# Kernel optimization log

Measured on AMD Instinct MI355X. Metric: run time of the kernel, lower is better.

## Reference

```python
import jax, jax.numpy as jnp
import numpy as np

B, C, H, NP, M = 32, 768, 12, 196, 64
D = C // H
GRID = 14  # sqrt(196)
NG = 1 + NP  # cls + patches = 197
EPS = 1e-5


def _ln(x, w, b):
    mu = x.mean(-1, keepdims=True)
    var = ((x - mu) ** 2).mean(-1, keepdims=True)
    return (x - mu) * jax.lax.rsqrt(var + EPS) * w + b


def setup_inputs() -> dict:
    key = jax.random.key(0)
    ks = jax.random.split(key, 14)
    std = 0.02
    return {
        "x": jax.random.normal(ks[0], (B, NG + M, C), dtype=jnp.float32),
        "ps": jax.random.uniform(ks[1], (B, M, 2), dtype=jnp.float32) * 224.0,
        "ns": jax.random.randint(ks[2], (B,), 1, M + 1, dtype=jnp.int32),
        "norm1_w": jnp.ones((C,), jnp.float32),
        "norm1_b": jnp.zeros((C,), jnp.float32),
        "qkv_w": jax.random.normal(ks[3], (3 * C, C), jnp.float32) * std,
        "proj_w": jax.random.normal(ks[4], (C, C), jnp.float32) * std,
        "proj_b": jnp.zeros((C,), jnp.float32),
        "norm2_w": jnp.ones((C,), jnp.float32),
        "norm2_b": jnp.zeros((C,), jnp.float32),
        "fc1_w": jax.random.normal(ks[5], (4 * C, C), jnp.float32) * std,
        "fc1_b": jnp.zeros((4 * C,), jnp.float32),
        "fc2_w": jax.random.normal(ks[6], (C, 4 * C), jnp.float32) * std,
        "fc2_b": jnp.zeros((C,), jnp.float32),
    }


def reference(x, ps, ns, norm1_w, norm1_b, qkv_w, proj_w, proj_b,
              norm2_w, norm2_b, fc1_w, fc1_b, fc2_w, fc2_b):
    Bn, Nt, Cd = x.shape  # Nt = 1 + 196 + M
    scale = D ** -0.5

    h = _ln(x, norm1_w, norm1_b)
    qkv = (h @ qkv_w.T).reshape(Bn, Nt, 3, H, D).transpose(2, 0, 3, 1, 4)  # [3,B,H,Nt,D]
    q, k, v = qkv[0], qkv[1], qkv[2]

    # ---- global attention over cls + patch tokens (first 197) ----
    attn = jnp.einsum('bhnd,bhmd->bhnm', q[:, :, :NG], k[:, :, :NG]) * scale
    attn = jax.nn.softmax(attn, axis=-1)
    xg = jnp.einsum('bhnm,bhmd->bhnd', attn, v[:, :, :NG])
    xg = xg.transpose(0, 2, 1, 3).reshape(Bn, NG, Cd)  # [B,197,C]

    # ---- keypoint bilinear-gather attention (get_single_filter_matrix) ----
    pos = ps / 16.0  # [B,M,2]; pos[...,1] -> row (dim 4), pos[...,0] -> col (dim 5)
    c0 = jnp.clip(jnp.floor(pos[..., 0]), 0, GRID - 1).astype(jnp.int32)
    c1 = jnp.clip(jnp.ceil(pos[..., 0]), 0, GRID - 1).astype(jnp.int32)
    r0 = jnp.clip(jnp.floor(pos[..., 1]), 0, GRID - 1).astype(jnp.int32)
    r1 = jnp.clip(jnp.ceil(pos[..., 1]), 0, GRID - 1).astype(jnp.int32)
    # neighbor order: top_left, top_right, bottom_left, bottom_right
    rows = jnp.stack([r0, r1, r0, r1], axis=-1)  # [B,M,4]
    cols = jnp.stack([c0, c0, c1, c1], axis=-1)
    flat = rows * GRID + cols  # [B,M,4] flat index into 196 patch tokens

    kp = k[:, :, 1:NG]  # [B,H,196,D]
    vp = v[:, :, 1:NG]
    idx = jnp.broadcast_to(flat.reshape(Bn, 1, M * 4, 1), (Bn, H, M * 4, D))
    knb = jnp.take_along_axis(kp, idx, axis=2).reshape(Bn, H, M, 4, D)
    vnb = jnp.take_along_axis(vp, idx, axis=2).reshape(Bn, H, M, 4, D)

    qk = q[:, :, NG:]  # keypoint queries [B,H,M,D]
    a = jnp.einsum('bhmd,bhmjd->bhmj', qk, knb)  # no scale, per original
    a = jax.nn.softmax(a, axis=-1)
    kout = jnp.einsum('bhmj,bhmjd->bhmd', a, vnb)
    kout = kout.transpose(0, 2, 1, 3).reshape(Bn, M, Cd)

    y = jnp.concatenate([xg, kout], axis=1) @ proj_w.T + proj_b
    x = x + y

    h2 = _ln(x, norm2_w, norm2_b)
    h2 = jax.nn.gelu(h2 @ fc1_w.T + fc1_b, approximate=False)
    x = x + (h2 @ fc2_w.T + fc2_b)
    return x
```

## Files before the change

kernel.cpp:

```cpp
#include <hip/hip_runtime.h>

typedef unsigned short u16;
typedef unsigned int u32;
typedef u16 u16x8 __attribute__((ext_vector_type(8)));
typedef u16 u16x4 __attribute__((ext_vector_type(4)));
typedef float f32x4 __attribute__((ext_vector_type(4)));
typedef __bf16 bf16x8 __attribute__((ext_vector_type(8)));

#define NHEAD 12
#define NT 261
#define NGL 197
#define CDIM 768
#define KT 14
#define PS_STRIDE 232
#define VT_STRIDE 232

__device__ __forceinline__ float bf2f(u16 u) {
    u32 x = ((u32)u) << 16;
    float f;
    __builtin_memcpy(&f, &x, 4);
    return f;
}
__device__ __forceinline__ u16 f2bf(float f) {
    u32 x;
    __builtin_memcpy(&x, &f, 4);
    x = (x + 0x7fffu + ((x >> 16) & 1u)) >> 16;
    return (u16)x;
}

#define GLD_LDS16(g, l) \
    __builtin_amdgcn_global_load_lds((const __attribute__((address_space(1))) void*)(g), \
                                     (__attribute__((address_space(3))) void*)(l), 16, 0, 0)
#define WAITV(n) asm volatile("s_waitcnt vmcnt(" #n ")" ::: "memory")
#define BARM() asm volatile("s_barrier" ::: "memory")

struct CvArgs {
    const float* in[4];
    u16* out[4];
    int n4[4];
};
__global__ __launch_bounds__(256) void convk4(CvArgs a) {
    int y = blockIdx.y;
    const float* in = a.in[y];
    u16* out = a.out[y];
    int n4 = a.n4[y];
    int i = blockIdx.x * 256 + threadIdx.x;
    if (i >= n4) return;
    float4 v = ((const float4*)in)[i];
    u16x4 o;
    o[0] = f2bf(v.x); o[1] = f2bf(v.y); o[2] = f2bf(v.z); o[3] = f2bf(v.w);
    ((u16x4*)out)[i] = o;
}

__global__ __launch_bounds__(256) void ln_k(const float* __restrict__ in, const float* __restrict__ w,
                                            const float* __restrict__ bia, u16* __restrict__ out) {
    int row = blockIdx.x;
    int tid = threadIdx.x;
    const float* r = in + (size_t)row * CDIM;
    float v0 = r[tid], v1 = r[tid + 256], v2 = r[tid + 512];
    float s = v0 + v1 + v2;
    float ss = v0 * v0 + v1 * v1 + v2 * v2;
#pragma unroll
    for (int off = 32; off; off >>= 1) {
        s += __shfl_xor(s, off);
        ss += __shfl_xor(ss, off);
    }
    __shared__ float ls[4], lss[4];
    int wv = tid >> 6;
    if ((tid & 63) == 0) { ls[wv] = s; lss[wv] = ss; }
    __syncthreads();
    s = ls[0] + ls[1] + ls[2] + ls[3];
    ss = lss[0] + lss[1] + lss[2] + lss[3];
    float mu = s * (1.f / 768.f);
    float var = ss * (1.f / 768.f) - mu * mu;
    float inv = rsqrtf(var + 1e-5f);
    u16* o = out + (size_t)row * CDIM;
    o[tid]       = f2bf((v0 - mu) * inv * w[tid]       + bia[tid]);
    o[tid + 256] = f2bf((v1 - mu) * inv * w[tid + 256] + bia[tid + 256]);
    o[tid + 512] = f2bf((v2 - mu) * inv * w[tid + 512] + bia[tid + 512]);
}

template <int EPI, int TM>
__global__ __launch_bounds__(TM * 2, 2) void gemm4(const u16* __restrict__ A, const u16* __restrict__ Bw,
                                                   int M, int N, int K, int nbn,
                                                   const float* __restrict__ bias,
                                                   const float* __restrict__ resid, void* __restrict__ outp) {
    constexpr int THREADS = TM * 2;
    constexpr int ROWSP = THREADS / 8;
    constexpr int NBI = 128 / ROWSP;
    constexpr int SLOT = TM * 64 + 8192;
    __shared__ __align__(16) u16 sm[2 * SLOT];
    const int tid = threadIdx.x;
    const int nwg = gridDim.x;
    const int q = nwg >> 3, r = nwg & 7;
    const int xcd = blockIdx.x & 7, within = blockIdx.x >> 3;
    const int id2 = (xcd < r ? xcd * (q + 1) : r * (q + 1) + (xcd - r) * q) + within;
    const int bm = id2 / nbn, bn = id2 % nbn;
    const int lane = tid & 63, wv = tid >> 6;
    const int wr = wv >> 1, wc = wv & 1;
    const int l15 = lane & 15, lg = lane >> 4;
    const int arow0 = bm * TM, brow0 = bn * 128;
    const int nt = K >> 6;

    const int srow = tid >> 3;
    const int sk = ((tid & 7) ^ (srow & 7)) * 8;
    const u16* gA[4];
    const u16* gB[NBI];
#pragma unroll
    for (int i = 0; i < 4; ++i) {
        int ar = arow0 + i * ROWSP + srow;
        if (ar >= M) ar = M - 1;
        gA[i] = A + (size_t)ar * K + sk;
    }
#pragma unroll
    for (int j = 0; j < NBI; ++j)
        gB[j] = Bw + (size_t)(brow0 + j * ROWSP + srow) * K + sk;

    auto STAGE = [&](int tt) {
        u16* sb = sm + (tt & 1) * SLOT;
        const size_t ko = (size_t)tt * 64;
#pragma unroll
        for (int i = 0; i < 4; ++i) GLD_LDS16(gA[i] + ko, sb + i * (ROWSP * 64) + tid * 8);
#pragma unroll
        for (int j = 0; j < NBI; ++j) GLD_LDS16(gB[j] + ko, sb + TM * 64 + j * (ROWSP * 64) + tid * 8);
    };

    f32x4 acc[4][4] = {};
    const int xb = l15 & 7;

    STAGE(0);
    for (int t = 0; t < nt; ++t) {
        if (t + 1 < nt) {
            STAGE(t + 1);
            if constexpr (TM == 256) { WAITV(6); } else { WAITV(8); }
        } else {
            WAITV(0);
        }
        BARM();
        const u16* sb = sm + (t & 1) * SLOT;
        bf16x8 af[4][2], bq[4][2];
#pragma unroll
        for (int mi = 0; mi < 4; ++mi)
#pragma unroll
            for (int kk = 0; kk < 2; ++kk)
                af[mi][kk] = *(const bf16x8*)(sb + (wr * 64 + mi * 16 + l15) * 64 + (((kk << 2) | lg) ^ xb) * 8);
#pragma unroll
        for (int ni = 0; ni < 4; ++ni)
#pragma unroll
            for (int kk = 0; kk < 2; ++kk)
                bq[ni][kk] = *(const bf16x8*)(sb + TM * 64 + (wc * 64 + ni * 16 + l15) * 64 + (((kk << 2) | lg) ^ xb) * 8);
#pragma unroll
        for (int mi = 0; mi < 4; ++mi)
#pragma unroll
            for (int ni = 0; ni < 4; ++ni) {
                acc[mi][ni] = __builtin_amdgcn_mfma_f32_16x16x32_bf16(af[mi][0], bq[ni][0], acc[mi][ni], 0, 0, 0);
                acc[mi][ni] = __builtin_amdgcn_mfma_f32_16x16x32_bf16(af[mi][1], bq[ni][1], acc[mi][ni], 0, 0, 0);
            }
        if (t + 2 < nt) BARM();
    }

#pragma unroll
    for (int mi = 0; mi < 4; ++mi) {
        int row0 = arow0 + wr * 64 + mi * 16 + lg * 4;
#pragma unroll
        for (int ni = 0; ni < 4; ++ni) {
            int col = brow0 + wc * 64 + ni * 16 + l15;
            float bb = (EPI == 0) ? 0.f : bias[col];
#pragma unroll
            for (int rr = 0; rr < 4; ++rr) {
                int row = row0 + rr;
                if (row < M) {
                    float v = acc[mi][ni][rr] + bb;
                    if (EPI == 2) {
                        float z = v + 0.044715f * v * v * v;
                        v = v / (1.f + __expf(-1.5957691216f * z));
                    }
                    if (EPI == 1) {
                        v += resid[(size_t)row * N + col];
                        ((float*)outp)[(size_t)row * N + col] = v;
                    } else {
                        ((u16*)outp)[(size_t)row * N + col] = f2bf(v);
                    }
                }
            }
        }
    }
}

__global__ __launch_bounds__(256) void attn_global_mfma(const u16* __restrict__ qkv, u16* __restrict__ Z) {
    __shared__ __align__(16) u16 lds0[4 * 16 * PS_STRIDE];
    __shared__ __align__(16) u16 Vt[64 * VT_STRIDE];
    const int tid = threadIdx.x;
    const int blk = blockIdx.x;
    const int qt = blk & 3;
    const int bh = blk >> 2;
    const int h = bh % NHEAD, b = bh / NHEAD;
    const int lane = tid & 63, wv = tid >> 6;
    const int l15 = lane & 15, lg = lane >> 4;
    const u16* base = qkv + (size_t)b * NT * 2304;

    for (int c = tid; c < 224 * 8; c += 256) {
        int row = c >> 3, ch = c & 7;
        u16x8 v = {};
        if (row < NGL) v = *(const u16x8*)(base + (size_t)row * 2304 + 768 + h * 64 + ch * 8);
        int byte = row * 128 + ((ch * 16) ^ ((row & 7) << 4));
        *(u16x8*)((char*)lds0 + byte) = v;
    }
    for (int c = tid; c < 112 * 8; c += 256) {
        int mp = c >> 3, dch = c & 7;
        int m0 = mp * 2;
        u16x8 a0 = {}, a1 = {};
        if (m0 < NGL)     a0 = *(const u16x8*)(base + (size_t)m0 * 2304 + 1536 + h * 64 + dch * 8);
        if (m0 + 1 < NGL) a1 = *(const u16x8*)(base + (size_t)(m0 + 1) * 2304 + 1536 + h * 64 + dch * 8);
#pragma unroll
        for (int j = 0; j < 8; ++j) {
            u32 pk = (u32)a0[j] | ((u32)a1[j] << 16);
            *(u32*)((char*)Vt + (size_t)(dch * 8 + j) * (VT_STRIDE * 2) + m0 * 2) = pk;
        }
    }
    const int q0 = qt * 64 + wv * 16;
    int qrow = q0 + l15; if (qrow > NGL - 1) qrow = NGL - 1;
    bf16x8 aq0 = *(const bf16x8*)(base + (size_t)qrow * 2304 + h * 64 + lg * 8);
    bf16x8 aq1 = *(const bf16x8*)(base + (size_t)qrow * 2304 + h * 64 + 32 + lg * 8);
    __syncthreads();

    f32x4 s[KT];
    const int sw = (l15 & 7) << 4;
#pragma unroll
    for (int t = 0; t < KT; ++t) {
        const char* krow = (const char*)lds0 + (t * 16 + l15) * 128;
        bf16x8 bk0 = *(const bf16x8*)(krow + ((lg * 16) ^ sw));
        bf16x8 bk1 = *(const bf16x8*)(krow + ((64 + lg * 16) ^ sw));
        f32x4 acc = {};
        acc = __builtin_amdgcn_mfma_f32_16x16x32_bf16(aq0, bk0, acc, 0, 0, 0);
        acc = __builtin_amdgcn_mfma_f32_16x16x32_bf16(aq1, bk1, acc, 0, 0, 0);
        s[t] = acc * 0.125f;
    }
    float mx[4] = {-1e30f, -1e30f, -1e30f, -1e30f};
#pragma unroll
    for (int t = 0; t < KT; ++t)
#pragma unroll
        for (int r = 0; r < 4; ++r) mx[r] = fmaxf(mx[r], s[t][r]);
#pragma unroll
    for (int off = 1; off < 16; off <<= 1)
#pragma unroll
        for (int r = 0; r < 4; ++r) mx[r] = fmaxf(mx[r], __shfl_xor(mx[r], off));
    float sum[4] = {};
#pragma unroll
    for (int t = 0; t < KT; ++t) {
        bool valid = (t * 16 + l15) < NGL;
#pragma unroll
        for (int r = 0; r < 4; ++r) {
            float e = valid ? __expf(s[t][r] - mx[r]) : 0.f;
            s[t][r] = e;
            sum[r] += e;
        }
    }
#pragma unroll
    for (int off = 1; off < 16; off <<= 1)
#pragma unroll
        for (int r = 0; r < 4; ++r) sum[r] += __shfl_xor(sum[r], off);
    float inv[4];
#pragma unroll
    for (int r = 0; r < 4; ++r) inv[r] = 1.f / sum[r];

    __syncthreads();
    u16* Pw = lds0 + wv * 16 * PS_STRIDE;
#pragma unroll
    for (int t = 0; t < KT; ++t)
#pragma unroll
        for (int r = 0; r < 4; ++r)
            Pw[(4 * lg + r) * PS_STRIDE + t * 16 + l15] = f2bf(s[t][r] * inv[r]);

    f32x4 o[4] = {};
#pragma unroll
    for (int ks = 0; ks < 7; ++ks) {
        bf16x8 pa = *(const bf16x8*)(Pw + l15 * PS_STRIDE + ks * 32 + lg * 8);
#pragma unroll
        for (int dt = 0; dt < 4; ++dt) {
            bf16x8 bv = *(const bf16x8*)((const char*)Vt + (size_t)(dt * 16 + l15) * (VT_STRIDE * 2) + ks * 64 + lg * 16);
            o[dt] = __builtin_amdgcn_mfma_f32_16x16x32_bf16(pa, bv, o[dt], 0, 0, 0);
        }
    }
#pragma unroll
    for (int dt = 0; dt < 4; ++dt)
#pragma unroll
        for (int r = 0; r < 4; ++r) {
            int q = q0 + 4 * lg + r;
            if (q < NGL) Z[((size_t)b * NT + q) * CDIM + h * 64 + dt * 16 + l15] = f2bf(o[dt][r]);
        }
}

__global__ __launch_bounds__(64) void attn_neigh(const u16* __restrict__ qkv, const float* __restrict__ ps,
                                                 u16* __restrict__ Z) {
    int blk = blockIdx.x;
    int b = blk >> 6, m = blk & 63;
    int lane = threadIdx.x;
    float px = ps[((size_t)b * 64 + m) * 2 + 0] * (1.f / 16.f);
    float py = ps[((size_t)b * 64 + m) * 2 + 1] * (1.f / 16.f);
    int c0 = min(max((int)floorf(px), 0), 13);
    int c1 = min(max((int)ceilf(px), 0), 13);
    int r0 = min(max((int)floorf(py), 0), 13);
    int r1 = min(max((int)ceilf(py), 0), 13);
    int tok[4];
    tok[0] = 1 + r0 * 14 + c0;
    tok[1] = 1 + r1 * 14 + c0;
    tok[2] = 1 + r0 * 14 + c1;
    tok[3] = 1 + r1 * 14 + c1;
    const size_t rowq = ((size_t)b * NT + NGL + m) * 2304;
#pragma unroll 1
    for (int h = 0; h < NHEAD; ++h) {
        float qv = bf2f(qkv[rowq + h * 64 + lane]);
        float a[4];
#pragma unroll
        for (int j = 0; j < 4; ++j) {
            float p = qv * bf2f(qkv[((size_t)b * NT + tok[j]) * 2304 + 768 + h * 64 + lane]);
#pragma unroll
            for (int off = 32; off; off >>= 1) p += __shfl_xor(p, off);
            a[j] = p;
        }
        float mx = fmaxf(fmaxf(a[0], a[1]), fmaxf(a[2], a[3]));
        float e0 = expf(a[0] - mx), e1 = expf(a[1] - mx), e2 = expf(a[2] - mx), e3 = expf(a[3] - mx);
        float inv = 1.f / (e0 + e1 + e2 + e3);
        float v0 = bf2f(qkv[((size_t)b * NT + tok[0]) * 2304 + 1536 + h * 64 + lane]);
        float v1 = bf2f(qkv[((size_t)b * NT + tok[1]) * 2304 + 1536 + h * 64 + lane]);
        float v2 = bf2f(qkv[((size_t)b * NT + tok[2]) * 2304 + 1536 + h * 64 + lane]);
        float v3 = bf2f(qkv[((size_t)b * NT + tok[3]) * 2304 + 1536 + h * 64 + lane]);
        float o = (e0 * v0 + e1 * v1 + e2 * v2 + e3 * v3) * inv;
        Z[((size_t)b * NT + NGL + m) * CDIM + h * 64 + lane] = f2bf(o);
    }
}

extern "C" void kernel_launch(void* const* d_in, const int* in_sizes, int n_in,
                              void* d_out, int out_size, void* d_ws, size_t ws_size,
                              hipStream_t stream) {
    const float* x      = (const float*)d_in[0];
    const float* ps     = (const float*)d_in[1];
    const float* n1w    = (const float*)d_in[3];
    const float* n1b    = (const float*)d_in[4];
    const float* qkv_w  = (const float*)d_in[5];
    const float* proj_w = (const float*)d_in[6];
    const float* proj_b = (const float*)d_in[7];
    const float* n2w    = (const float*)d_in[8];
    const float* n2b    = (const float*)d_in[9];
    const float* fc1_w  = (const float*)d_in[10];
    const float* fc1_b  = (const float*)d_in[11];
    const float* fc2_w  = (const float*)d_in[12];
    const float* fc2_b  = (const float*)d_in[13];

    char* ws = (char*)d_ws;
    const int M = 32 * NT;
    u16* hbuf  = (u16*)ws;
    u16* qkvb  = (u16*)(ws + 12828672);
    u16* Zb    = (u16*)(ws + 12828672 + 38486016);
    u16* Gb    = (u16*)(ws + 12828672);
    float* x1  = (float*)(ws + 64143360);
    u16* wq    = (u16*)(ws + 89800704);
    u16* wp    = wq + 2304 * 768;
    u16* w1    = wp + 768 * 768;
    u16* w2    = w1 + 3072 * 768;

    CvArgs cv;
    cv.in[0] = qkv_w;  cv.out[0] = wq; cv.n4[0] = 2304 * 768 / 4;
    cv.in[1] = proj_w; cv.out[1] = wp; cv.n4[1] = 768 * 768 / 4;
    cv.in[2] = fc1_w;  cv.out[2] = w1; cv.n4[2] = 3072 * 768 / 4;
    cv.in[3] = fc2_w;  cv.out[3] = w2; cv.n4[3] = 768 * 3072 / 4;
    convk4<<<dim3((3072 * 768 / 4 + 255) / 256, 4), 256, 0, stream>>>(cv);

    ln_k<<<M, 256, 0, stream>>>(x, n1w, n1b, hbuf);
    gemm4<0, 256><<<33 * 18, 512, 0, stream>>>(hbuf, wq, M, 2304, 768, 18, nullptr, nullptr, qkvb);
    attn_global_mfma<<<32 * NHEAD * 4, 256, 0, stream>>>(qkvb, Zb);
    attn_neigh<<<32 * 64, 64, 0, stream>>>(qkvb, ps, Zb);
    gemm4<1, 128><<<66 * 6, 256, 0, stream>>>(Zb, wp, M, 768, 768, 6, proj_b, x, x1);
    ln_k<<<M, 256, 0, stream>>>(x1, n2w, n2b, hbuf);
    gemm4<2, 256><<<33 * 24, 512, 0, stream>>>(hbuf, w1, M, 3072, 768, 24, fc1_b, nullptr, Gb);
    gemm4<1, 128><<<66 * 6, 256, 0, stream>>>(Gb, w2, M, 768, 3072, 6, fc2_b, x1, (float*)d_out);
}
```

Measured before the change: 309.1 us.

## Use 256x256 tiles for QKV and FC1 GEMMs with 8-wave blocks

Adds a gemm5 kernel that computes 256x256 output tiles with 8 waves arranged 2x4. Each wave holds 8x4 accumulator fragments, which roughly doubles operand reuse per LDS load compared with the 256x128 tile. It is used for the QKV and FC1 GEMMs, halving their grid sizes. The cost is more registers and 128KB of double-buffered LDS per block, which lowers occupancy and leaves fewer blocks to fill the GPU.

```diff
diff --git a/kernel.cpp b/kernel.cpp
--- a/kernel.cpp
+++ b/kernel.cpp
@@ -80,15 +80,107 @@
     o[tid + 512] = f2bf((v2 - mu) * inv * w[tid + 512] + bia[tid + 512]);
 }
 
-template <int EPI, int TM>
-__global__ __launch_bounds__(TM * 2, 2) void gemm4(const u16* __restrict__ A, const u16* __restrict__ Bw,
-                                                   int M, int N, int K, int nbn,
-                                                   const float* __restrict__ bias,
-                                                   const float* __restrict__ resid, void* __restrict__ outp) {
-    constexpr int THREADS = TM * 2;
-    constexpr int ROWSP = THREADS / 8;
-    constexpr int NBI = 128 / ROWSP;
-    constexpr int SLOT = TM * 64 + 8192;
+template <int EPI>
+__global__ __launch_bounds__(512, 2) void gemm5(const u16* __restrict__ A, const u16* __restrict__ Bw,
+                                                int M, int N, int K, int nbn,
+                                                const float* __restrict__ bias,
+                                                void* __restrict__ outp) {
+    __shared__ __align__(16) u16 sm[2][32768];
+    const int tid = threadIdx.x;
+    const int nwg = gridDim.x;
+    const int q = nwg >> 3, r = nwg & 7;
+    const int xcd = blockIdx.x & 7, within = blockIdx.x >> 3;
+    const int id2 = (xcd < r ? xcd * (q + 1) : r * (q + 1) + (xcd - r) * q) + within;
+    const int bm = id2 / nbn, bn = id2 % nbn;
+    const int lane = tid & 63, wv = tid >> 6;
+    const int wr = wv >> 2, wc = wv & 3;
+    const int l15 = lane & 15, lg = lane >> 4;
+    const int arow0 = bm * 256, brow0 = bn * 256;
+    const int nt = K >> 6;
+
+    const int srow = tid >> 3;
+    const int sk = ((tid & 7) ^ (srow & 7)) * 8;
+    const u16* gA[4];
+    const u16* gB[4];
+#pragma unroll
+    for (int i = 0; i < 4; ++i) {
+        int ar = arow0 + i * 64 + srow;
+        if (ar >= M) ar = M - 1;
+        gA[i] = A + (size_t)ar * K + sk;
+        gB[i] = Bw + (size_t)(brow0 + i * 64 + srow) * K + sk;
+    }
+
+    auto STAGE = [&](int tt) {
+        u16* sb = sm[tt & 1];
+        const size_t ko = (size_t)tt * 64;
+#pragma unroll
+        for (int i = 0; i < 4; ++i) GLD_LDS16(gA[i] + ko, sb + i * 4096 + tid * 8);
+#pragma unroll
+        for (int i = 0; i < 4; ++i) GLD_LDS16(gB[i] + ko, sb + 16384 + i * 4096 + tid * 8);
+    };
+
+    f32x4 acc[8][4] = {};
+    const int xb = l15 & 7;
+
+    STAGE(0);
+    for (int t = 0; t < nt; ++t) {
+        if (t + 1 < nt) {
+            STAGE(t + 1);
+            WAITV(8);
+        } else {
+            WAITV(0);
+        }
+        BARM();
+        const u16* sb = sm[t & 1];
+        bf16x8 bq[4][2];
+#pragma unroll
+        for (int ni = 0; ni < 4; ++ni)
+#pragma unroll
+            for (int kk = 0; kk < 2; ++kk)
+                bq[ni][kk] = *(const bf16x8*)(sb + 16384 + (wc * 64 + ni * 16 + l15) * 64 + (((kk << 2) | lg) ^ xb) * 8);
+#pragma unroll
+        for (int mi = 0; mi < 8; ++mi) {
+            const u16* arow = sb + (wr * 128 + mi * 16 + l15) * 64;
+            bf16x8 a0 = *(const bf16x8*)(arow + ((lg ^ xb) * 8));
+            bf16x8 a1 = *(const bf16x8*)(arow + (((4 | lg) ^ xb) * 8));
+#pragma unroll
+            for (int ni = 0; ni < 4; ++ni) {
+                acc[mi][ni] = __builtin_amdgcn_mfma_f32_16x16x32_bf16(a0, bq[ni][0], acc[mi][ni], 0, 0, 0);
+                acc[mi][ni] = __builtin_amdgcn_mfma_f32_16x16x32_bf16(a1, bq[ni][1], acc[mi][ni], 0, 0, 0);
+            }
+        }
+        if (t + 2 < nt) BARM();
+    }
+
+#pragma unroll
+    for (int mi = 0; mi < 8; ++mi) {
+        int row0 = arow0 + wr * 128 + mi * 16 + lg * 4;
+#pragma unroll
+        for (int ni = 0; ni < 4; ++ni) {
+            int col = brow0 + wc * 64 + ni * 16 + l15;
+            float bb = (EPI == 0) ? 0.f : bias[col];
+#pragma unroll
+            for (int rr = 0; rr < 4; ++rr) {
+                int row = row0 + rr;
+                if (row < M) {
+                    float v = acc[mi][ni][rr] + bb;
+                    if (EPI == 2) {
+                        float z = v + 0.044715f * v * v * v;
+                        v = v / (1.f + __expf(-1.5957691216f * z));
+                    }
+                    ((u16*)outp)[(size_t)row * N + col] = f2bf(v);
+                }
+            }
+        }
+    }
+}
+
+template <int EPI>
+__global__ __launch_bounds__(256, 2) void gemm4n(const u16* __restrict__ A, const u16* __restrict__ Bw,
+                                                 int M, int N, int K, int nbn,
+                                                 const float* __restrict__ bias,
+                                                 const float* __restrict__ resid, void* __restrict__ outp) {
+    constexpr int SLOT = 128 * 64 + 8192;
     __shared__ __align__(16) u16 sm[2 * SLOT];
     const int tid = threadIdx.x;
     const int nwg = gridDim.x;
@@ -99,30 +191,28 @@
     const int lane = tid & 63, wv = tid >> 6;
     const int wr = wv >> 1, wc = wv & 1;
     const int l15 = lane & 15, lg = lane >> 4;
-    const int arow0 = bm * TM, brow0 = bn * 128;
+    const int arow0 = bm * 128, brow0 = bn * 128;
     const int nt = K >> 6;
 
     const int srow = tid >> 3;
     const int sk = ((tid & 7) ^ (srow & 7)) * 8;
     const u16* gA[4];
-    const u16* gB[NBI];
+    const u16* gB[4];
 #pragma unroll
     for (int i = 0; i < 4; ++i) {
-        int ar = arow0 + i * ROWSP + srow;
+        int ar = arow0 + i * 32 + srow;
         if (ar >= M) ar = M - 1;
         gA[i] = A + (size_t)ar * K + sk;
-    }
-#pragma unroll
-    for (int j = 0; j < NBI; ++j)
-        gB[j] = Bw + (size_t)(brow0 + j * ROWSP + srow) * K + sk;
+        gB[i] = Bw + (size_t)(brow0 + i * 32 + srow) * K + sk;
+    }
 
     auto STAGE = [&](int tt) {
         u16* sb = sm + (tt & 1) * SLOT;
         const size_t ko = (size_t)tt * 64;
 #pragma unroll
-        for (int i = 0; i < 4; ++i) GLD_LDS16(gA[i] + ko, sb + i * (ROWSP * 64) + tid * 8);
-#pragma unroll
-        for (int j = 0; j < NBI; ++j) GLD_LDS16(gB[j] + ko, sb + TM * 64 + j * (ROWSP * 64) + tid * 8);
+        for (int i = 0; i < 4; ++i) GLD_LDS16(gA[i] + ko, sb + i * 2048 + tid * 8);
+#pragma unroll
+        for (int i = 0; i < 4; ++i) GLD_LDS16(gB[i] + ko, sb + 8192 + i * 2048 + tid * 8);
     };
 
     f32x4 acc[4][4] = {};
@@ -132,7 +222,7 @@
     for (int t = 0; t < nt; ++t) {
         if (t + 1 < nt) {
             STAGE(t + 1);
-            if constexpr (TM == 256) { WAITV(6); } else { WAITV(8); }
+            WAITV(8);
         } else {
             WAITV(0);
         }
@@ -148,7 +238,7 @@
         for (int ni = 0; ni < 4; ++ni)
 #pragma unroll
             for (int kk = 0; kk < 2; ++kk)
-                bq[ni][kk] = *(const bf16x8*)(sb + TM * 64 + (wc * 64 + ni * 16 + l15) * 64 + (((kk << 2) | lg) ^ xb) * 8);
+                bq[ni][kk] = *(const bf16x8*)(sb + 8192 + (wc * 64 + ni * 16 + l15) * 64 + (((kk << 2) | lg) ^ xb) * 8);
 #pragma unroll
         for (int mi = 0; mi < 4; ++mi)
 #pragma unroll
@@ -165,22 +255,13 @@
 #pragma unroll
         for (int ni = 0; ni < 4; ++ni) {
             int col = brow0 + wc * 64 + ni * 16 + l15;
-            float bb = (EPI == 0) ? 0.f : bias[col];
+            float bb = bias[col];
 #pragma unroll
             for (int rr = 0; rr < 4; ++rr) {
                 int row = row0 + rr;
                 if (row < M) {
-                    float v = acc[mi][ni][rr] + bb;
-                    if (EPI == 2) {
-                        float z = v + 0.044715f * v * v * v;
-                        v = v / (1.f + __expf(-1.5957691216f * z));
-                    }
-                    if (EPI == 1) {
-                        v += resid[(size_t)row * N + col];
-                        ((float*)outp)[(size_t)row * N + col] = v;
-                    } else {
-                        ((u16*)outp)[(size_t)row * N + col] = f2bf(v);
-                    }
+                    float v = acc[mi][ni][rr] + bb + resid[(size_t)row * N + col];
+                    ((float*)outp)[(size_t)row * N + col] = v;
                 }
             }
         }
@@ -368,11 +449,11 @@
     convk4<<<dim3((3072 * 768 / 4 + 255) / 256, 4), 256, 0, stream>>>(cv);
 
     ln_k<<<M, 256, 0, stream>>>(x, n1w, n1b, hbuf);
-    gemm4<0, 256><<<33 * 18, 512, 0, stream>>>(hbuf, wq, M, 2304, 768, 18, nullptr, nullptr, qkvb);
+    gemm5<0><<<33 * 9, 512, 0, stream>>>(hbuf, wq, M, 2304, 768, 9, nullptr, qkvb);
     attn_global_mfma<<<32 * NHEAD * 4, 256, 0, stream>>>(qkvb, Zb);
     attn_neigh<<<32 * 64, 64, 0, stream>>>(qkvb, ps, Zb);
-    gemm4<1, 128><<<66 * 6, 256, 0, stream>>>(Zb, wp, M, 768, 768, 6, proj_b, x, x1);
+    gemm4n<1><<<66 * 6, 256, 0, stream>>>(Zb, wp, M, 768, 768, 6, proj_b, x, x1);
     ln_k<<<M, 256, 0, stream>>>(x1, n2w, n2b, hbuf);
-    gemm4<2, 256><<<33 * 24, 512, 0, stream>>>(hbuf, w1, M, 3072, 768, 24, fc1_b, nullptr, Gb);
-    gemm4<1, 128><<<66 * 6, 256, 0, stream>>>(Gb, w2, M, 768, 3072, 6, fc2_b, x1, (float*)d_out);
-}
+    gemm5<2><<<33 * 12, 512, 0, stream>>>(hbuf, w1, M, 3072, 768, 12, fc1_b, Gb);
+    gemm4n<1><<<66 * 6, 256, 0, stream>>>(Gb, w2, M, 768, 3072, 6, fc2_b, x1, (float*)d_out);
+}
```

Measured after the change: 308.7 us. Within noise of the previous version (-0.1%).

## Triple-buffer GEMM pipeline with split A/B staging and K-half ping-pong

Applied to the files above, without the earlier changes.

Replaces the double-buffered GEMM with a three-slot LDS pipeline that prefetches two K-tiles ahead. A and B loads for a future tile are issued in separate halves, interleaved with two MFMA phases, each guarded by barriers and raised wave priority. All GEMMs, including the 768-wide projection and fc2, now use 256-row tiles with 512 threads, which halves the number of workgroups for those. The extra LDS (about 144KB per block) and extra barriers may reduce occupancy, and the smaller grid for the N=768 GEMMs may underfill the GPU.

```diff
diff --git a/kernel.cpp b/kernel.cpp
--- a/kernel.cpp
+++ b/kernel.cpp
@@ -32,6 +32,7 @@
     __builtin_amdgcn_global_load_lds((const __attribute__((address_space(1))) void*)(g), \
                                      (__attribute__((address_space(3))) void*)(l), 16, 0, 0)
 #define WAITV(n) asm volatile("s_waitcnt vmcnt(" #n ")" ::: "memory")
+#define LGKM0()  asm volatile("s_waitcnt lgkmcnt(0)" ::: "memory")
 #define BARM() asm volatile("s_barrier" ::: "memory")
 
 struct CvArgs {
@@ -80,16 +81,13 @@
     o[tid + 512] = f2bf((v2 - mu) * inv * w[tid + 512] + bia[tid + 512]);
 }
 
-template <int EPI, int TM>
-__global__ __launch_bounds__(TM * 2, 2) void gemm4(const u16* __restrict__ A, const u16* __restrict__ Bw,
-                                                   int M, int N, int K, int nbn,
-                                                   const float* __restrict__ bias,
-                                                   const float* __restrict__ resid, void* __restrict__ outp) {
-    constexpr int THREADS = TM * 2;
-    constexpr int ROWSP = THREADS / 8;
-    constexpr int NBI = 128 / ROWSP;
-    constexpr int SLOT = TM * 64 + 8192;
-    __shared__ __align__(16) u16 sm[2 * SLOT];
+template <int EPI>
+__global__ __launch_bounds__(512, 2) void gemm6(const u16* __restrict__ A, const u16* __restrict__ Bw,
+                                                int M, int N, int K, int nbn,
+                                                const float* __restrict__ bias,
+                                                const float* __restrict__ resid, void* __restrict__ outp) {
+    constexpr int BUF = 24576;
+    __shared__ __align__(16) u16 sm[3 * BUF];
     const int tid = threadIdx.x;
     const int nwg = gridDim.x;
     const int q = nwg >> 3, r = nwg & 7;
@@ -99,64 +97,81 @@
     const int lane = tid & 63, wv = tid >> 6;
     const int wr = wv >> 1, wc = wv & 1;
     const int l15 = lane & 15, lg = lane >> 4;
-    const int arow0 = bm * TM, brow0 = bn * 128;
+    const int arow0 = bm * 256, brow0 = bn * 128;
     const int nt = K >> 6;
 
     const int srow = tid >> 3;
     const int sk = ((tid & 7) ^ (srow & 7)) * 8;
     const u16* gA[4];
-    const u16* gB[NBI];
+    const u16* gB[2];
 #pragma unroll
     for (int i = 0; i < 4; ++i) {
-        int ar = arow0 + i * ROWSP + srow;
+        int ar = arow0 + i * 64 + srow;
         if (ar >= M) ar = M - 1;
         gA[i] = A + (size_t)ar * K + sk;
     }
 #pragma unroll
-    for (int j = 0; j < NBI; ++j)
-        gB[j] = Bw + (size_t)(brow0 + j * ROWSP + srow) * K + sk;
-
-    auto STAGE = [&](int tt) {
-        u16* sb = sm + (tt & 1) * SLOT;
+    for (int j = 0; j < 2; ++j)
+        gB[j] = Bw + (size_t)(brow0 + j * 64 + srow) * K + sk;
+
+    auto STAGE_A = [&](int tt) {
+        u16* sb = sm + (tt % 3) * BUF;
         const size_t ko = (size_t)tt * 64;
 #pragma unroll
-        for (int i = 0; i < 4; ++i) GLD_LDS16(gA[i] + ko, sb + i * (ROWSP * 64) + tid * 8);
-#pragma unroll
-        for (int j = 0; j < NBI; ++j) GLD_LDS16(gB[j] + ko, sb + TM * 64 + j * (ROWSP * 64) + tid * 8);
+        for (int i = 0; i < 4; ++i) GLD_LDS16(gA[i] + ko, sb + i * 4096 + tid * 8);
+    };
+    auto STAGE_B = [&](int tt) {
+        u16* sb = sm + (tt % 3) * BUF;
+        const size_t ko = (size_t)tt * 64;
+#pragma unroll
+        for (int j = 0; j < 2; ++j) GLD_LDS16(gB[j] + ko, sb + 16384 + j * 4096 + tid * 8);
     };
 
     f32x4 acc[4][4] = {};
     const int xb = l15 & 7;
 
-    STAGE(0);
+    STAGE_A(0); STAGE_B(0);
+    STAGE_A(1); STAGE_B(1);
     for (int t = 0; t < nt; ++t) {
-        if (t + 1 < nt) {
-            STAGE(t + 1);
-            if constexpr (TM == 256) { WAITV(6); } else { WAITV(8); }
-        } else {
-            WAITV(0);
-        }
+        if (t + 1 < nt) { WAITV(6); } else { WAITV(0); }
         BARM();
-        const u16* sb = sm + (t & 1) * SLOT;
-        bf16x8 af[4][2], bq[4][2];
+        const u16* sb = sm + (t % 3) * BUF;
+        const bool pre = (t + 2 < nt);
+        if (pre) STAGE_A(t + 2);
+        bf16x8 af0[4], bq0[4];
 #pragma unroll
         for (int mi = 0; mi < 4; ++mi)
-#pragma unroll
-            for (int kk = 0; kk < 2; ++kk)
-                af[mi][kk] = *(const bf16x8*)(sb + (wr * 64 + mi * 16 + l15) * 64 + (((kk << 2) | lg) ^ xb) * 8);
+            af0[mi] = *(const bf16x8*)(sb + (wr * 64 + mi * 16 + l15) * 64 + ((lg ^ xb) << 3));
 #pragma unroll
         for (int ni = 0; ni < 4; ++ni)
-#pragma unroll
-            for (int kk = 0; kk < 2; ++kk)
-                bq[ni][kk] = *(const bf16x8*)(sb + TM * 64 + (wc * 64 + ni * 16 + l15) * 64 + (((kk << 2) | lg) ^ xb) * 8);
+            bq0[ni] = *(const bf16x8*)(sb + 16384 + (wc * 64 + ni * 16 + l15) * 64 + ((lg ^ xb) << 3));
+        LGKM0();
+        BARM();
+        __builtin_amdgcn_s_setprio(1);
 #pragma unroll
         for (int mi = 0; mi < 4; ++mi)
 #pragma unroll
-            for (int ni = 0; ni < 4; ++ni) {
-                acc[mi][ni] = __builtin_amdgcn_mfma_f32_16x16x32_bf16(af[mi][0], bq[ni][0], acc[mi][ni], 0, 0, 0);
-                acc[mi][ni] = __builtin_amdgcn_mfma_f32_16x16x32_bf16(af[mi][1], bq[ni][1], acc[mi][ni], 0, 0, 0);
-            }
-        if (t + 2 < nt) BARM();
+            for (int ni = 0; ni < 4; ++ni)
+                acc[mi][ni] = __builtin_amdgcn_mfma_f32_16x16x32_bf16(af0[mi], bq0[ni], acc[mi][ni], 0, 0, 0);
+        __builtin_amdgcn_s_setprio(0);
+        BARM();
+        if (pre) STAGE_B(t + 2);
+        bf16x8 af1[4], bq1[4];
+#pragma unroll
+        for (int mi = 0; mi < 4; ++mi)
+            af1[mi] = *(const bf16x8*)(sb + (wr * 64 + mi * 16 + l15) * 64 + (((4 | lg) ^ xb) << 3));
+#pragma unroll
+        for (int ni = 0; ni < 4; ++ni)
+            bq1[ni] = *(const bf16x8*)(sb + 16384 + (wc * 64 + ni * 16 + l15) * 64 + (((4 | lg) ^ xb) << 3));
+        LGKM0();
+        BARM();
+        __builtin_amdgcn_s_setprio(1);
+#pragma unroll
+        for (int mi = 0; mi < 4; ++mi)
+#pragma unroll
+            for (int ni = 0; ni < 4; ++ni)
+                acc[mi][ni] = __builtin_amdgcn_mfma_f32_16x16x32_bf16(af1[mi], bq1[ni], acc[mi][ni], 0, 0, 0);
+        __builtin_amdgcn_s_setprio(0);
     }
 
 #pragma unroll
@@ -368,11 +383,11 @@
     convk4<<<dim3((3072 * 768 / 4 + 255) / 256, 4), 256, 0, stream>>>(cv);
 
     ln_k<<<M, 256, 0, stream>>>(x, n1w, n1b, hbuf);
-    gemm4<0, 256><<<33 * 18, 512, 0, stream>>>(hbuf, wq, M, 2304, 768, 18, nullptr, nullptr, qkvb);
+    gemm6<0><<<33 * 18, 512, 0, stream>>>(hbuf, wq, M, 2304, 768, 18, nullptr, nullptr, qkvb);
     attn_global_mfma<<<32 * NHEAD * 4, 256, 0, stream>>>(qkvb, Zb);
     attn_neigh<<<32 * 64, 64, 0, stream>>>(qkvb, ps, Zb);
-    gemm4<1, 128><<<66 * 6, 256, 0, stream>>>(Zb, wp, M, 768, 768, 6, proj_b, x, x1);
+    gemm6<1><<<33 * 6, 512, 0, stream>>>(Zb, wp, M, 768, 768, 6, proj_b, x, x1);
     ln_k<<<M, 256, 0, stream>>>(x1, n2w, n2b, hbuf);
-    gemm4<2, 256><<<33 * 24, 512, 0, stream>>>(hbuf, w1, M, 3072, 768, 24, fc1_b, nullptr, Gb);
-    gemm4<1, 128><<<66 * 6, 256, 0, stream>>>(Gb, w2, M, 768, 3072, 6, fc2_b, x1, (float*)d_out);
-}
+    gemm6<2><<<33 * 24, 512, 0, stream>>>(hbuf, w1, M, 3072, 768, 24, fc1_b, nullptr, Gb);
+    gemm6<1><<<33 * 6, 512, 0, stream>>>(Gb, w2, M, 768, 3072, 6, fc2_b, x1, (float*)d_out);
+}
```

After: 327.4 us. 5.9% more time.
